# Kernel tuning notes

Measured on AMD Instinct MI355X. Metric: run time of the kernel, lower is better.

## Reference

```python
import math
import jax, jax.numpy as jnp
import numpy as np

B, T, D = 2, 2048, 1024
NUM_HEADS = 16
NUM_KV_HEADS = 4
HEAD_DIM = 64
ROPE_THETA = 500000.0


def precompute_freqs_cis(dim, seq_len, theta):
    freqs = 1.0 / theta ** (jnp.arange(0, dim, 2).astype(jnp.float32) / dim)
    freqs = jnp.outer(jnp.arange(seq_len), freqs)  # [T, dim//2]
    return jnp.cos(freqs), jnp.sin(freqs)


def apply_rotary_emb(xq, xk, cos, sin):
    # xq:[B,T,H,Dh], cos/sin:[T,Dh//2] -> broadcast as [1,T,1,Dh//2]
    c = cos[None, :, None, :]
    s = sin[None, :, None, :]

    def rot(x):
        xr = x.reshape(*x.shape[:-1], -1, 2)
        x0, x1 = xr[..., 0], xr[..., 1]
        return jnp.stack([x0 * c - x1 * s, x1 * c + x0 * s], axis=-1).reshape(x.shape)

    return rot(xq), rot(xk)


def setup_inputs() -> dict:
    key = jax.random.key(0)
    ks = jax.random.split(key, 5)
    x = jax.random.normal(ks[0], (B, T, D), dtype=jnp.float32)
    # causal mask [B,1,T,T]
    mask = jnp.broadcast_to(jnp.tril(jnp.ones((T, T), dtype=bool))[None, None], (B, 1, T, T))
    sq = 1.0 / math.sqrt(D)
    Wq = jax.random.normal(ks[1], (D, NUM_HEADS * HEAD_DIM), dtype=jnp.float32) * sq
    Wk = jax.random.normal(ks[2], (D, NUM_KV_HEADS * HEAD_DIM), dtype=jnp.float32) * sq
    Wv = jax.random.normal(ks[3], (D, NUM_KV_HEADS * HEAD_DIM), dtype=jnp.float32) * sq
    Wo = jax.random.normal(ks[4], (NUM_HEADS * HEAD_DIM, D), dtype=jnp.float32) * (1.0 / math.sqrt(NUM_HEADS * HEAD_DIM))
    return {"x": x, "mask": mask, "Wq": Wq, "Wk": Wk, "Wv": Wv, "Wo": Wo}


def reference(x, mask, Wq, Wk, Wv, Wo):
    b, t, _ = x.shape
    n_rep = NUM_HEADS // NUM_KV_HEADS
    q = (x @ Wq).reshape(b, t, NUM_HEADS, HEAD_DIM)
    k = (x @ Wk).reshape(b, t, NUM_KV_HEADS, HEAD_DIM)
    v = (x @ Wv).reshape(b, t, NUM_KV_HEADS, HEAD_DIM)
    cos, sin = precompute_freqs_cis(HEAD_DIM, t, ROPE_THETA)
    q, k = apply_rotary_emb(q, k, cos, sin)
    k = jnp.repeat(k, n_rep, axis=2)
    v = jnp.repeat(v, n_rep, axis=2)
    q = q.transpose(0, 2, 1, 3)  # [B,H,T,Dh]
    k = k.transpose(0, 2, 1, 3)
    v = v.transpose(0, 2, 1, 3)
    scale = 1.0 / math.sqrt(HEAD_DIM)
    attn = jnp.einsum('bhqd,bhkd->bhqk', q, k) * scale
    attn = jnp.where(mask, attn, -1e9)
    attn = jax.nn.softmax(attn, axis=-1)
    out = jnp.einsum('bhqk,bhkd->bhqd', attn, v)
    out = out.transpose(0, 2, 1, 3).reshape(b, t, -1)
    return out @ Wo
```

## Files before the change

kernel.cpp:

```cpp
#include <hip/hip_runtime.h>
#include <hip/hip_bf16.h>

#define B_  2
#define T_  2048
#define D_  1024
#define H_  16
#define KH_ 4
#define DH_ 64

typedef __attribute__((ext_vector_type(8))) short bf16x8;
typedef __attribute__((ext_vector_type(4))) float f32x4;

#define QSCALE 0.18033688011112043f

#if defined(__has_builtin)
#  if __has_builtin(__builtin_amdgcn_exp2f)
#    define EXP2F(x) __builtin_amdgcn_exp2f(x)
#  endif
#endif
#ifndef EXP2F
#  define EXP2F(x) exp2f(x)
#endif

__device__ __forceinline__ unsigned short f2bf(float f) {
  union { float f; unsigned int u; } v; v.f = f;
  return (unsigned short)((v.u + 0x7FFFu + ((v.u >> 16) & 1u)) >> 16);
}
__device__ __forceinline__ unsigned int pk2(float a, float b) {
  union { __hip_bfloat162 h2; unsigned int u; } v;
  v.h2 = __float22bfloat162_rn(make_float2(a, b));
  return v.u;
}


__global__ __launch_bounds__(256) void prep_kernel(
    const float* __restrict__ x,  const float* __restrict__ Wq,
    const float* __restrict__ Wk, const float* __restrict__ Wv,
    const float* __restrict__ Wo,
    short* __restrict__ xb, short* __restrict__ WT, short* __restrict__ WoT,
    float2* __restrict__ tbl) {
  __shared__ short Ts[64 * 72];
  const int bid = blockIdx.x, tid = threadIdx.x;

  if (bid < 2048) {
    const size_t i8 = ((size_t)bid * 256 + tid) * 8;
    const float4 a = *(const float4*)&x[i8];
    const float4 b = *(const float4*)&x[i8 + 4];
    uint4 p; p.x = pk2(a.x, a.y); p.y = pk2(a.z, a.w);
    p.z = pk2(b.x, b.y); p.w = pk2(b.z, b.w);
    *(uint4*)&xb[i8] = p;
  } else if (bid < 2688) {
    const bool isW = bid < 2432;
    const int idx = isW ? (bid - 2048) : (bid - 2432);
    const int n0 = (idx >> 4) * 64, k0 = (idx & 15) * 64;
    const float* src; int ncols, c0; short* dst;
    if (isW) {
      dst = WT;
      if (n0 < 1024)      { src = Wq; ncols = 1024; c0 = n0; }
      else if (n0 < 1280) { src = Wk; ncols = 256;  c0 = n0 - 1024; }
      else                { src = Wv; ncols = 256;  c0 = n0 - 1280; }
    } else { dst = WoT; src = Wo; ncols = 1024; c0 = n0; }
    for (int i = tid; i < 1024; i += 256) {
      const int kr = i >> 4, c4 = (i & 15) << 2;
      const int kc = isW ? kr : ((kr & 15) * 4 + (kr >> 4));
      const float4 w = *(const float4*)&src[(size_t)(k0 + kr) * ncols + c0 + c4];
      Ts[(c4 + 0) * 72 + kc] = (short)f2bf(w.x);
      Ts[(c4 + 1) * 72 + kc] = (short)f2bf(w.y);
      Ts[(c4 + 2) * 72 + kc] = (short)f2bf(w.z);
      Ts[(c4 + 3) * 72 + kc] = (short)f2bf(w.w);
    }
    __syncthreads();
    for (int c = tid; c < 512; c += 256) {
      const int nr = c >> 3, c8 = (c & 7) * 8;
      *(bf16x8*)&dst[(size_t)(n0 + nr) * 1024 + k0 + c8] =
          *(const bf16x8*)&Ts[nr * 72 + c8];
    }
  } else {
    const int e = (bid - 2688) * 256 + tid;
    const int t = e >> 5, i2 = e & 31;
    const float freq = exp2f(-(float)(2 * i2) * (18.931568569324174f / 64.0f));
    float sn, cs; sincosf((float)t * freq, &sn, &cs);
    tbl[e] = make_float2(cs, sn);
  }
}

__global__ __launch_bounds__(256) void qkv_mfma_kernel(
    const short* __restrict__ xb, const short* __restrict__ WT,
    const float2* __restrict__ tbl,
    short* __restrict__ qo, short* __restrict__ ko, short* __restrict__ vt) {
  __shared__ short Xs[128 * 136];
  __shared__ short Wt[64 * 136];
  const int tid = threadIdx.x;
  const int lane = tid & 63, w = tid >> 6;
  const int lm = lane & 15, quad = lane >> 4;
  const int m0 = blockIdx.x * 128;
  const int n0 = blockIdx.y * 64;

  f32x4 acc[2][4];
  #pragma unroll
  for (int sm = 0; sm < 2; ++sm)
    #pragma unroll
    for (int ct = 0; ct < 4; ++ct) acc[sm][ct] = (f32x4){0.f, 0.f, 0.f, 0.f};

  bf16x8 px[8], pw[4];
  #pragma unroll
  for (int u = 0; u < 8; ++u) {
    const int c = tid + u * 256, row = c >> 4, c8 = (c & 15) * 8;
    px[u] = *(const bf16x8*)&xb[(size_t)(m0 + row) * 1024 + c8];
  }
  #pragma unroll
  for (int u = 0; u < 4; ++u) {
    const int c = tid + u * 256, row = c >> 4, c8 = (c & 15) * 8;
    pw[u] = *(const bf16x8*)&WT[(size_t)(n0 + row) * 1024 + c8];
  }

  for (int kt = 0; kt < 8; ++kt) {
    __syncthreads();
    #pragma unroll
    for (int u = 0; u < 8; ++u) {
      const int c = tid + u * 256, row = c >> 4, c8 = (c & 15) * 8;
      *(bf16x8*)&Xs[row * 136 + c8] = px[u];
    }
    #pragma unroll
    for (int u = 0; u < 4; ++u) {
      const int c = tid + u * 256, row = c >> 4, c8 = (c & 15) * 8;
      *(bf16x8*)&Wt[row * 136 + c8] = pw[u];
    }
    __syncthreads();
    if (kt < 7) {
      #pragma unroll
      for (int u = 0; u < 8; ++u) {
        const int c = tid + u * 256, row = c >> 4, c8 = (c & 15) * 8;
        px[u] = *(const bf16x8*)&xb[(size_t)(m0 + row) * 1024 + (kt + 1) * 128 + c8];
      }
      #pragma unroll
      for (int u = 0; u < 4; ++u) {
        const int c = tid + u * 256, row = c >> 4, c8 = (c & 15) * 8;
        pw[u] = *(const bf16x8*)&WT[(size_t)(n0 + row) * 1024 + (kt + 1) * 128 + c8];
      }
    }
    #pragma unroll
    for (int s = 0; s < 4; ++s) {
      bf16x8 bfr[4];
      #pragma unroll
      for (int ct = 0; ct < 4; ++ct)
        bfr[ct] = *(const bf16x8*)&Wt[(ct * 16 + lm) * 136 + s * 32 + quad * 8];
      #pragma unroll
      for (int sm = 0; sm < 2; ++sm) {
        const bf16x8 a =
            *(const bf16x8*)&Xs[(w * 32 + sm * 16 + lm) * 136 + s * 32 + quad * 8];
        #pragma unroll
        for (int ct = 0; ct < 4; ++ct)
          acc[sm][ct] =
              __builtin_amdgcn_mfma_f32_16x16x32_bf16(a, bfr[ct], acc[sm][ct], 0, 0, 0);
      }
    }
  }

  if (n0 < 1280) {
    const bool isQ = n0 < 1024;
    short* outp = isQ ? qo : ko;
    const int base = isQ ? n0 : n0 - 1024;
    const int nh = isQ ? H_ : KH_;
    const int hh = base >> 6;
    const float post = isQ ? QSCALE : 1.0f;
    #pragma unroll
    for (int sm = 0; sm < 2; ++sm)
      #pragma unroll
      for (int r = 0; r < 4; ++r) {
        const int row = m0 + w * 32 + sm * 16 + quad * 4 + r;
        const int b = row >> 11, t = row & 2047;
        float v4[4];
        #pragma unroll
        for (int ct = 0; ct < 4; ++ct) {
          float val = acc[sm][ct][r];
          const float other = __shfl_xor(val, 1);
          const int ci = ct * 16 + lm;
          const float2 cs = tbl[t * 32 + (ci >> 1)];
          val = ((ci & 1) == 0) ? (val * cs.x - other * cs.y)
                                : (val * cs.x + other * cs.y);
          v4[ct] = val * post;
        }
        uint2 st; st.x = pk2(v4[0], v4[1]); st.y = pk2(v4[2], v4[3]);
        *(uint2*)&outp[((size_t)(b * nh + hh) * T_ + t) * DH_ + lm * 4] = st;
      }
  } else {
    __syncthreads();
    #pragma unroll
    for (int sm = 0; sm < 2; ++sm)
      #pragma unroll
      for (int r = 0; r < 4; ++r)
        #pragma unroll
        for (int ct = 0; ct < 4; ++ct)
          Xs[(w * 32 + sm * 16 + quad * 4 + r) * 72 + ct * 16 + lm] =
              (short)f2bf(acc[sm][ct][r]);
    __syncthreads();
    const int kh = (n0 - 1280) >> 6;
    const int b = m0 >> 11, t0 = m0 & 2047;
    short* vb = vt + (size_t)(b * KH_ + kh) * DH_ * T_;
    for (int c = tid; c < 1024; c += 256) {
      const int d = c >> 4, c8 = (c & 15) * 8;
      short tmp[8];
      #pragma unroll
      for (int j = 0; j < 8; ++j) {
        const int s = c8 + j, sg = s & 63;
        const int tok = (s & 64) + ((sg & 3) << 4) + (sg >> 2);
        tmp[j] = Xs[tok * 72 + d];
      }
      *(bf16x8*)&vb[(size_t)d * T_ + t0 + c8] = *(bf16x8*)tmp;
    }
  }
}

__global__ __launch_bounds__(256) void attn_mfma_kernel(
    const short* __restrict__ q, const short* __restrict__ k,
    const short* __restrict__ vt, short* __restrict__ att) {
  __shared__ short Qs[64 * 72];
  __shared__ short Ks[128 * 72];
  __shared__ short Vts[64 * 136];
  __shared__ short Ps0[64 * 72];
  __shared__ short Ps1[64 * 72];

  const int h = blockIdx.y, b = blockIdx.z;
  const int kh = h >> 2;
  const int tid = threadIdx.x;
  const int lane = tid & 63, w = tid >> 6;
  const int lm = lane & 15, quad = lane >> 4;

  const short* qb = q + (size_t)(b * H_ + h) * T_ * DH_;
  const short* kb = k + (size_t)(b * KH_ + kh) * T_ * DH_;
  const short* vb = vt + (size_t)(b * KH_ + kh) * DH_ * T_;

  bf16x8 ones;
  #pragma unroll
  for (int i = 0; i < 8; ++i) ones[i] = (short)0x3F80;

  for (int half = 0; half < 2; ++half) {
    const int qt = half ? (31 - blockIdx.x) : blockIdx.x;
    const int q0 = qt * 64;

    __syncthreads();
    for (int c = tid; c < 512; c += 256) {
      const int row = c >> 3, c8 = (c & 7) * 8;
      *(bf16x8*)&Qs[row * 72 + c8] =
          *(const bf16x8*)&qb[(size_t)(q0 + row) * 64 + c8];
    }

    bf16x8 pk[4], pv[4];
    #pragma unroll
    for (int u = 0; u < 4; ++u) {
      const int c = tid + u * 256;
      const int row = c >> 3, c8 = (c & 7) * 8;
      pk[u] = *(const bf16x8*)&kb[(size_t)row * 64 + c8];
      const int d = c >> 4, c16 = (c & 15) * 8;
      pv[u] = *(const bf16x8*)&vb[(size_t)d * T_ + c16];
    }
    __syncthreads();
    bf16x8 aq[2];
    #pragma unroll
    for (int s = 0; s < 2; ++s)
      aq[s] = *(const bf16x8*)&Qs[(w * 16 + lm) * 72 + s * 32 + quad * 8];

    f32x4 oacc[4], lacc;
    #pragma unroll
    for (int i = 0; i < 4; ++i) oacc[i] = (f32x4){0.f, 0.f, 0.f, 0.f};
    lacc = (f32x4){0.f, 0.f, 0.f, 0.f};

    auto step = [&](int j, bool diag, short* Ps) {
      f32x4 sacc[4];
      #pragma unroll
      for (int i = 0; i < 4; ++i) sacc[i] = (f32x4){0.f, 0.f, 0.f, 0.f};
      #pragma unroll
      for (int s = 0; s < 2; ++s) {
        #pragma unroll
        for (int ct = 0; ct < 4; ++ct) {
          const bf16x8 bb =
              *(const bf16x8*)&Ks[(j * 64 + ct * 16 + lm) * 72 + s * 32 + quad * 8];
          sacc[ct] = __builtin_amdgcn_mfma_f32_16x16x32_bf16(aq[s], bb, sacc[ct], 0, 0, 0);
        }
      }
      if (diag) {
        #pragma unroll
        for (int r = 0; r < 4; ++r) {
          const int qi = w * 16 + quad * 4 + r;
          float p[4];
          #pragma unroll
          for (int ct = 0; ct < 4; ++ct) {
            float pv2 = EXP2F(sacc[ct][r]);
            if ((ct * 16 + lm) > qi) pv2 = 0.f;
            p[ct] = pv2;
          }
          uint2 pw2; pw2.x = pk2(p[0], p[1]); pw2.y = pk2(p[2], p[3]);
          *(uint2*)&Ps[qi * 72 + lm * 4] = pw2;
        }
      } else {
        #pragma unroll
        for (int r = 0; r < 4; ++r) {
          const int qi = w * 16 + quad * 4 + r;
          uint2 pw2;
          pw2.x = pk2(EXP2F(sacc[0][r]), EXP2F(sacc[1][r]));
          pw2.y = pk2(EXP2F(sacc[2][r]), EXP2F(sacc[3][r]));
          *(uint2*)&Ps[qi * 72 + lm * 4] = pw2;
        }
      }
      #pragma unroll
      for (int s = 0; s < 2; ++s) {
        const bf16x8 pa = *(const bf16x8*)&Ps[(w * 16 + lm) * 72 + s * 32 + quad * 8];
        lacc = __builtin_amdgcn_mfma_f32_16x16x32_bf16(pa, ones, lacc, 0, 0, 0);
        #pragma unroll
        for (int ct = 0; ct < 4; ++ct) {
          const bf16x8 vfr = *(const bf16x8*)&Vts[(ct * 16 + lm) * 136 +
                                                  j * 64 + s * 32 + quad * 8];
          oacc[ct] = __builtin_amdgcn_mfma_f32_16x16x32_bf16(pa, vfr, oacc[ct], 0, 0, 0);
        }
      }
    };

    auto stage = [&](int r2) {
      __syncthreads();
      #pragma unroll
      for (int u = 0; u < 4; ++u) {
        const int c = tid + u * 256;
        const int row = c >> 3, c8 = (c & 7) * 8;
        *(bf16x8*)&Ks[row * 72 + c8] = pk[u];
        const int d = c >> 4, c16 = (c & 15) * 8;
        *(bf16x8*)&Vts[d * 136 + c16] = pv[u];
      }
      __syncthreads();
      const int r2n = (r2 + 2 <= 30) ? (r2 + 2) : 30;
      #pragma unroll
      for (int u = 0; u < 4; ++u) {
        const int c = tid + u * 256;
        const int row = c >> 3, c8 = (c & 7) * 8;
        pk[u] = *(const bf16x8*)&kb[(size_t)(r2n * 64 + row) * 64 + c8];
        const int d = c >> 4, c16 = (c & 15) * 8;
        pv[u] = *(const bf16x8*)&vb[(size_t)d * T_ + r2n * 64 + c16];
      }
    };

    int r2 = 0;
    for (; r2 + 1 <= qt; r2 += 2) {
      stage(r2);
      step(0, false, Ps0);
      step(1, r2 + 1 == qt, Ps1);
    }
    if (r2 == qt) {
      stage(r2);
      step(0, true, Ps0);
    }

    #pragma unroll
    for (int r = 0; r < 4; ++r) {
      const int qrow = q0 + w * 16 + quad * 4 + r;
      const float inv = 1.f / lacc[r];
      uint2 st;
      st.x = pk2(oacc[0][r] * inv, oacc[1][r] * inv);
      st.y = pk2(oacc[2][r] * inv, oacc[3][r] * inv);
      *(uint2*)&att[((size_t)b * T_ + qrow) * 1024 + h * 64 + lm * 4] = st;
    }
  }
}

__global__ __launch_bounds__(256) void outproj_mfma_kernel(
    const short* __restrict__ att, const short* __restrict__ WoT,
    float* __restrict__ out) {
  __shared__ short Xs[128 * 136];
  __shared__ short Wt[64 * 136];
  const int tid = threadIdx.x;
  const int lane = tid & 63, w = tid >> 6;
  const int lm = lane & 15, quad = lane >> 4;
  const int m0 = blockIdx.x * 128;
  const int n0 = blockIdx.y * 64;

  f32x4 acc[2][4];
  #pragma unroll
  for (int sm = 0; sm < 2; ++sm)
    #pragma unroll
    for (int ct = 0; ct < 4; ++ct) acc[sm][ct] = (f32x4){0.f, 0.f, 0.f, 0.f};

  bf16x8 px[8], pw[4];
  #pragma unroll
  for (int u = 0; u < 8; ++u) {
    const int c = tid + u * 256, row = c >> 4, c8 = (c & 15) * 8;
    px[u] = *(const bf16x8*)&att[(size_t)(m0 + row) * 1024 + c8];
  }
  #pragma unroll
  for (int u = 0; u < 4; ++u) {
    const int c = tid + u * 256, row = c >> 4, c8 = (c & 15) * 8;
    pw[u] = *(const bf16x8*)&WoT[(size_t)(n0 + row) * 1024 + c8];
  }

  for (int kt = 0; kt < 8; ++kt) {
    __syncthreads();
    #pragma unroll
    for (int u = 0; u < 8; ++u) {
      const int c = tid + u * 256, row = c >> 4, c8 = (c & 15) * 8;
      *(bf16x8*)&Xs[row * 136 + c8] = px[u];
    }
    #pragma unroll
    for (int u = 0; u < 4; ++u) {
      const int c = tid + u * 256, row = c >> 4, c8 = (c & 15) * 8;
      *(bf16x8*)&Wt[row * 136 + c8] = pw[u];
    }
    __syncthreads();
    if (kt < 7) {
      #pragma unroll
      for (int u = 0; u < 8; ++u) {
        const int c = tid + u * 256, row = c >> 4, c8 = (c & 15) * 8;
        px[u] = *(const bf16x8*)&att[(size_t)(m0 + row) * 1024 + (kt + 1) * 128 + c8];
      }
      #pragma unroll
      for (int u = 0; u < 4; ++u) {
        const int c = tid + u * 256, row = c >> 4, c8 = (c & 15) * 8;
        pw[u] = *(const bf16x8*)&WoT[(size_t)(n0 + row) * 1024 + (kt + 1) * 128 + c8];
      }
    }
    #pragma unroll
    for (int s = 0; s < 4; ++s) {
      bf16x8 bfr[4];
      #pragma unroll
      for (int ct = 0; ct < 4; ++ct)
        bfr[ct] = *(const bf16x8*)&Wt[(ct * 16 + lm) * 136 + s * 32 + quad * 8];
      #pragma unroll
      for (int sm = 0; sm < 2; ++sm) {
        const bf16x8 a =
            *(const bf16x8*)&Xs[(w * 32 + sm * 16 + lm) * 136 + s * 32 + quad * 8];
        #pragma unroll
        for (int ct = 0; ct < 4; ++ct)
          acc[sm][ct] =
              __builtin_amdgcn_mfma_f32_16x16x32_bf16(a, bfr[ct], acc[sm][ct], 0, 0, 0);
      }
    }
  }

  #pragma unroll
  for (int sm = 0; sm < 2; ++sm)
    #pragma unroll
    for (int r = 0; r < 4; ++r) {
      const int row = m0 + w * 32 + sm * 16 + quad * 4 + r;
      #pragma unroll
      for (int ct = 0; ct < 4; ++ct)
        out[(size_t)row * 1024 + n0 + ct * 16 + lm] = acc[sm][ct][r];
    }
}

extern "C" void kernel_launch(void* const* d_in, const int* in_sizes, int n_in,
                              void* d_out, int out_size, void* d_ws, size_t ws_size,
                              hipStream_t stream) {
  const float* x  = (const float*)d_in[0];
  const float* Wq = (const float*)d_in[2];
  const float* Wk = (const float*)d_in[3];
  const float* Wv = (const float*)d_in[4];
  const float* Wo = (const float*)d_in[5];
  float* out = (float*)d_out;

  short* xb   = (short*)d_ws;
  short* WT   = xb  + (size_t)4194304;
  short* WoT  = WT  + (size_t)1572864;
  short* qb   = WoT + (size_t)1048576;
  short* kb   = qb  + (size_t)4194304;
  short* vtb  = kb  + (size_t)1048576;
  short* attb = vtb + (size_t)1048576;
  float2* tbl = (float2*)(attb + (size_t)4194304);

  prep_kernel<<<dim3(2944), dim3(256), 0, stream>>>(
      x, Wq, Wk, Wv, Wo, xb, WT, WoT, tbl);
  qkv_mfma_kernel<<<dim3(32, 24), dim3(256), 0, stream>>>(xb, WT, tbl, qb, kb, vtb);
  attn_mfma_kernel<<<dim3(16, H_, B_), dim3(256), 0, stream>>>(qb, kb, vtb, attb);
  outproj_mfma_kernel<<<dim3(32, 16), dim3(256), 0, stream>>>(attb, WoT, out);
}
```

Before: 173.0 us.

## Use direct global-to-LDS loads with XOR swizzle and reschedule attention grid

The QKV and output-projection GEMMs now load tiles with global_load_lds straight into an XOR-swizzled, unpadded shared buffer instead of staging through registers. This removes the register prefetch, and with it the overlap of the next tile's loads with compute, because each k-step waits on vmcnt(0). The attention kernel drops the paired-query-tile loop and instead launches one block per query tile on a flat 1024-block grid ordered heaviest-first. It also loads Q fragments directly from global, and adds s_setprio around MFMA sections to favor matrix issue across waves.

```diff
diff --git a/kernel.cpp b/kernel.cpp
--- a/kernel.cpp
+++ b/kernel.cpp
@@ -30,6 +30,12 @@
   union { __hip_bfloat162 h2; unsigned int u; } v;
   v.h2 = __float22bfloat162_rn(make_float2(a, b));
   return v.u;
+}
+
+__device__ __forceinline__ void g2l16(const void* g, void* l) {
+  __builtin_amdgcn_global_load_lds(
+      (const __attribute__((address_space(1))) void*)g,
+      (__attribute__((address_space(3))) void*)l, 16, 0, 0);
 }
 
 
@@ -88,11 +94,13 @@
     const short* __restrict__ xb, const short* __restrict__ WT,
     const float2* __restrict__ tbl,
     short* __restrict__ qo, short* __restrict__ ko, short* __restrict__ vt) {
-  __shared__ short Xs[128 * 136];
-  __shared__ short Wt[64 * 136];
+  __shared__ short Xs[128 * 128];
+  __shared__ short Wt[64 * 128];
   const int tid = threadIdx.x;
   const int lane = tid & 63, w = tid >> 6;
   const int lm = lane & 15, quad = lane >> 4;
+  const int lr = lane >> 4;
+  const int lb = lane & 15;
   const int m0 = blockIdx.x * 128;
   const int n0 = blockIdx.y * 64;
 
@@ -102,53 +110,35 @@
     #pragma unroll
     for (int ct = 0; ct < 4; ++ct) acc[sm][ct] = (f32x4){0.f, 0.f, 0.f, 0.f};
 
-  bf16x8 px[8], pw[4];
-  #pragma unroll
-  for (int u = 0; u < 8; ++u) {
-    const int c = tid + u * 256, row = c >> 4, c8 = (c & 15) * 8;
-    px[u] = *(const bf16x8*)&xb[(size_t)(m0 + row) * 1024 + c8];
-  }
-  #pragma unroll
-  for (int u = 0; u < 4; ++u) {
-    const int c = tid + u * 256, row = c >> 4, c8 = (c & 15) * 8;
-    pw[u] = *(const bf16x8*)&WT[(size_t)(n0 + row) * 1024 + c8];
-  }
-
   for (int kt = 0; kt < 8; ++kt) {
     __syncthreads();
     #pragma unroll
     for (int u = 0; u < 8; ++u) {
-      const int c = tid + u * 256, row = c >> 4, c8 = (c & 15) * 8;
-      *(bf16x8*)&Xs[row * 136 + c8] = px[u];
+      const int r = (w * 8 + u) * 4 + lr;
+      const int sb = lb ^ (r & 7);
+      g2l16(&xb[(size_t)(m0 + r) * 1024 + kt * 128 + sb * 8],
+            &Xs[(w * 8 + u) * 512]);
     }
     #pragma unroll
     for (int u = 0; u < 4; ++u) {
-      const int c = tid + u * 256, row = c >> 4, c8 = (c & 15) * 8;
-      *(bf16x8*)&Wt[row * 136 + c8] = pw[u];
-    }
-    __syncthreads();
-    if (kt < 7) {
-      #pragma unroll
-      for (int u = 0; u < 8; ++u) {
-        const int c = tid + u * 256, row = c >> 4, c8 = (c & 15) * 8;
-        px[u] = *(const bf16x8*)&xb[(size_t)(m0 + row) * 1024 + (kt + 1) * 128 + c8];
-      }
-      #pragma unroll
-      for (int u = 0; u < 4; ++u) {
-        const int c = tid + u * 256, row = c >> 4, c8 = (c & 15) * 8;
-        pw[u] = *(const bf16x8*)&WT[(size_t)(n0 + row) * 1024 + (kt + 1) * 128 + c8];
-      }
-    }
+      const int r = (w * 4 + u) * 4 + lr;
+      const int sb = lb ^ (r & 7);
+      g2l16(&WT[(size_t)(n0 + r) * 1024 + kt * 128 + sb * 8],
+            &Wt[(w * 4 + u) * 512]);
+    }
+    asm volatile("s_waitcnt vmcnt(0)" ::: "memory");
+    __syncthreads();
     #pragma unroll
     for (int s = 0; s < 4; ++s) {
       bf16x8 bfr[4];
       #pragma unroll
       for (int ct = 0; ct < 4; ++ct)
-        bfr[ct] = *(const bf16x8*)&Wt[(ct * 16 + lm) * 136 + s * 32 + quad * 8];
+        bfr[ct] = *(const bf16x8*)&Wt[(ct * 16 + lm) * 128 +
+                                      (((s * 4 + quad) ^ (lm & 7)) << 3)];
       #pragma unroll
       for (int sm = 0; sm < 2; ++sm) {
-        const bf16x8 a =
-            *(const bf16x8*)&Xs[(w * 32 + sm * 16 + lm) * 136 + s * 32 + quad * 8];
+        const bf16x8 a = *(const bf16x8*)&Xs[(w * 32 + sm * 16 + lm) * 128 +
+                                             (((s * 4 + quad) ^ (lm & 7)) << 3)];
         #pragma unroll
         for (int ct = 0; ct < 4; ++ct)
           acc[sm][ct] =
@@ -215,17 +205,20 @@
 __global__ __launch_bounds__(256) void attn_mfma_kernel(
     const short* __restrict__ q, const short* __restrict__ k,
     const short* __restrict__ vt, short* __restrict__ att) {
-  __shared__ short Qs[64 * 72];
   __shared__ short Ks[128 * 72];
   __shared__ short Vts[64 * 136];
   __shared__ short Ps0[64 * 72];
   __shared__ short Ps1[64 * 72];
 
-  const int h = blockIdx.y, b = blockIdx.z;
+  const int bx = blockIdx.x;
+  const int qt = 31 - (bx >> 5);
+  const int hb = bx & 31;
+  const int h = hb >> 1, b = hb & 1;
   const int kh = h >> 2;
   const int tid = threadIdx.x;
   const int lane = tid & 63, w = tid >> 6;
   const int lm = lane & 15, quad = lane >> 4;
+  const int q0 = qt * 64;
 
   const short* qb = q + (size_t)(b * H_ + h) * T_ * DH_;
   const short* kb = k + (size_t)(b * KH_ + kh) * T_ * DH_;
@@ -235,140 +228,134 @@
   #pragma unroll
   for (int i = 0; i < 8; ++i) ones[i] = (short)0x3F80;
 
-  for (int half = 0; half < 2; ++half) {
-    const int qt = half ? (31 - blockIdx.x) : blockIdx.x;
-    const int q0 = qt * 64;
-
-    __syncthreads();
-    for (int c = tid; c < 512; c += 256) {
-      const int row = c >> 3, c8 = (c & 7) * 8;
-      *(bf16x8*)&Qs[row * 72 + c8] =
-          *(const bf16x8*)&qb[(size_t)(q0 + row) * 64 + c8];
-    }
-
-    bf16x8 pk[4], pv[4];
+  bf16x8 aq[2];
+  #pragma unroll
+  for (int s = 0; s < 2; ++s)
+    aq[s] = *(const bf16x8*)&qb[(size_t)(q0 + w * 16 + lm) * 64 + s * 32 + quad * 8];
+
+  bf16x8 pk[4], pv[4];
+  #pragma unroll
+  for (int u = 0; u < 4; ++u) {
+    const int c = tid + u * 256;
+    const int row = c >> 3, c8 = (c & 7) * 8;
+    pk[u] = *(const bf16x8*)&kb[(size_t)row * 64 + c8];
+    const int d = c >> 4, c16 = (c & 15) * 8;
+    pv[u] = *(const bf16x8*)&vb[(size_t)d * T_ + c16];
+  }
+
+  f32x4 oacc[4], lacc;
+  #pragma unroll
+  for (int i = 0; i < 4; ++i) oacc[i] = (f32x4){0.f, 0.f, 0.f, 0.f};
+  lacc = (f32x4){0.f, 0.f, 0.f, 0.f};
+
+  auto step = [&](int j, bool diag, short* Ps) {
+    f32x4 sacc[4];
+    #pragma unroll
+    for (int i = 0; i < 4; ++i) sacc[i] = (f32x4){0.f, 0.f, 0.f, 0.f};
+    __builtin_amdgcn_s_setprio(1);
+    #pragma unroll
+    for (int s = 0; s < 2; ++s) {
+      #pragma unroll
+      for (int ct = 0; ct < 4; ++ct) {
+        const bf16x8 bb =
+            *(const bf16x8*)&Ks[(j * 64 + ct * 16 + lm) * 72 + s * 32 + quad * 8];
+        sacc[ct] = __builtin_amdgcn_mfma_f32_16x16x32_bf16(aq[s], bb, sacc[ct], 0, 0, 0);
+      }
+    }
+    __builtin_amdgcn_s_setprio(0);
+    if (diag) {
+      #pragma unroll
+      for (int r = 0; r < 4; ++r) {
+        const int qi = w * 16 + quad * 4 + r;
+        float p[4];
+        #pragma unroll
+        for (int ct = 0; ct < 4; ++ct) {
+          float pv2 = EXP2F(sacc[ct][r]);
+          if ((ct * 16 + lm) > qi) pv2 = 0.f;
+          p[ct] = pv2;
+        }
+        uint2 pw2; pw2.x = pk2(p[0], p[1]); pw2.y = pk2(p[2], p[3]);
+        *(uint2*)&Ps[qi * 72 + lm * 4] = pw2;
+      }
+    } else {
+      #pragma unroll
+      for (int r = 0; r < 4; ++r) {
+        const int qi = w * 16 + quad * 4 + r;
+        uint2 pw2;
+        pw2.x = pk2(EXP2F(sacc[0][r]), EXP2F(sacc[1][r]));
+        pw2.y = pk2(EXP2F(sacc[2][r]), EXP2F(sacc[3][r]));
+        *(uint2*)&Ps[qi * 72 + lm * 4] = pw2;
+      }
+    }
+    __builtin_amdgcn_s_setprio(1);
+    #pragma unroll
+    for (int s = 0; s < 2; ++s) {
+      const bf16x8 pa = *(const bf16x8*)&Ps[(w * 16 + lm) * 72 + s * 32 + quad * 8];
+      lacc = __builtin_amdgcn_mfma_f32_16x16x32_bf16(pa, ones, lacc, 0, 0, 0);
+      #pragma unroll
+      for (int ct = 0; ct < 4; ++ct) {
+        const bf16x8 vfr = *(const bf16x8*)&Vts[(ct * 16 + lm) * 136 +
+                                                j * 64 + s * 32 + quad * 8];
+        oacc[ct] = __builtin_amdgcn_mfma_f32_16x16x32_bf16(pa, vfr, oacc[ct], 0, 0, 0);
+      }
+    }
+    __builtin_amdgcn_s_setprio(0);
+  };
+
+  auto stage = [&](int r2) {
+    __syncthreads();
     #pragma unroll
     for (int u = 0; u < 4; ++u) {
       const int c = tid + u * 256;
       const int row = c >> 3, c8 = (c & 7) * 8;
-      pk[u] = *(const bf16x8*)&kb[(size_t)row * 64 + c8];
+      *(bf16x8*)&Ks[row * 72 + c8] = pk[u];
       const int d = c >> 4, c16 = (c & 15) * 8;
-      pv[u] = *(const bf16x8*)&vb[(size_t)d * T_ + c16];
-    }
-    __syncthreads();
-    bf16x8 aq[2];
-    #pragma unroll
-    for (int s = 0; s < 2; ++s)
-      aq[s] = *(const bf16x8*)&Qs[(w * 16 + lm) * 72 + s * 32 + quad * 8];
-
-    f32x4 oacc[4], lacc;
-    #pragma unroll
-    for (int i = 0; i < 4; ++i) oacc[i] = (f32x4){0.f, 0.f, 0.f, 0.f};
-    lacc = (f32x4){0.f, 0.f, 0.f, 0.f};
-
-    auto step = [&](int j, bool diag, short* Ps) {
-      f32x4 sacc[4];
-      #pragma unroll
-      for (int i = 0; i < 4; ++i) sacc[i] = (f32x4){0.f, 0.f, 0.f, 0.f};
-      #pragma unroll
-      for (int s = 0; s < 2; ++s) {
-        #pragma unroll
-        for (int ct = 0; ct < 4; ++ct) {
-          const bf16x8 bb =
-              *(const bf16x8*)&Ks[(j * 64 + ct * 16 + lm) * 72 + s * 32 + quad * 8];
-          sacc[ct] = __builtin_amdgcn_mfma_f32_16x16x32_bf16(aq[s], bb, sacc[ct], 0, 0, 0);
-        }
-      }
-      if (diag) {
-        #pragma unroll
-        for (int r = 0; r < 4; ++r) {
-          const int qi = w * 16 + quad * 4 + r;
-          float p[4];
-          #pragma unroll
-          for (int ct = 0; ct < 4; ++ct) {
-            float pv2 = EXP2F(sacc[ct][r]);
-            if ((ct * 16 + lm) > qi) pv2 = 0.f;
-            p[ct] = pv2;
-          }
-          uint2 pw2; pw2.x = pk2(p[0], p[1]); pw2.y = pk2(p[2], p[3]);
-          *(uint2*)&Ps[qi * 72 + lm * 4] = pw2;
-        }
-      } else {
-        #pragma unroll
-        for (int r = 0; r < 4; ++r) {
-          const int qi = w * 16 + quad * 4 + r;
-          uint2 pw2;
-          pw2.x = pk2(EXP2F(sacc[0][r]), EXP2F(sacc[1][r]));
-          pw2.y = pk2(EXP2F(sacc[2][r]), EXP2F(sacc[3][r]));
-          *(uint2*)&Ps[qi * 72 + lm * 4] = pw2;
-        }
-      }
-      #pragma unroll
-      for (int s = 0; s < 2; ++s) {
-        const bf16x8 pa = *(const bf16x8*)&Ps[(w * 16 + lm) * 72 + s * 32 + quad * 8];
-        lacc = __builtin_amdgcn_mfma_f32_16x16x32_bf16(pa, ones, lacc, 0, 0, 0);
-        #pragma unroll
-        for (int ct = 0; ct < 4; ++ct) {
-          const bf16x8 vfr = *(const bf16x8*)&Vts[(ct * 16 + lm) * 136 +
-                                                  j * 64 + s * 32 + quad * 8];
-          oacc[ct] = __builtin_amdgcn_mfma_f32_16x16x32_bf16(pa, vfr, oacc[ct], 0, 0, 0);
-        }
-      }
-    };
-
-    auto stage = [&](int r2) {
-      __syncthreads();
-      #pragma unroll
-      for (int u = 0; u < 4; ++u) {
-        const int c = tid + u * 256;
-        const int row = c >> 3, c8 = (c & 7) * 8;
-        *(bf16x8*)&Ks[row * 72 + c8] = pk[u];
-        const int d = c >> 4, c16 = (c & 15) * 8;
-        *(bf16x8*)&Vts[d * 136 + c16] = pv[u];
-      }
-      __syncthreads();
-      const int r2n = (r2 + 2 <= 30) ? (r2 + 2) : 30;
-      #pragma unroll
-      for (int u = 0; u < 4; ++u) {
-        const int c = tid + u * 256;
-        const int row = c >> 3, c8 = (c & 7) * 8;
-        pk[u] = *(const bf16x8*)&kb[(size_t)(r2n * 64 + row) * 64 + c8];
-        const int d = c >> 4, c16 = (c & 15) * 8;
-        pv[u] = *(const bf16x8*)&vb[(size_t)d * T_ + r2n * 64 + c16];
-      }
-    };
-
-    int r2 = 0;
-    for (; r2 + 1 <= qt; r2 += 2) {
-      stage(r2);
-      step(0, false, Ps0);
-      step(1, r2 + 1 == qt, Ps1);
-    }
-    if (r2 == qt) {
-      stage(r2);
-      step(0, true, Ps0);
-    }
-
-    #pragma unroll
-    for (int r = 0; r < 4; ++r) {
-      const int qrow = q0 + w * 16 + quad * 4 + r;
-      const float inv = 1.f / lacc[r];
-      uint2 st;
-      st.x = pk2(oacc[0][r] * inv, oacc[1][r] * inv);
-      st.y = pk2(oacc[2][r] * inv, oacc[3][r] * inv);
-      *(uint2*)&att[((size_t)b * T_ + qrow) * 1024 + h * 64 + lm * 4] = st;
-    }
+      *(bf16x8*)&Vts[d * 136 + c16] = pv[u];
+    }
+    __syncthreads();
+    const int r2n = (r2 + 2 <= qt) ? (r2 + 2) : r2;
+    #pragma unroll
+    for (int u = 0; u < 4; ++u) {
+      const int c = tid + u * 256;
+      const int row = c >> 3, c8 = (c & 7) * 8;
+      pk[u] = *(const bf16x8*)&kb[(size_t)(r2n * 64 + row) * 64 + c8];
+      const int d = c >> 4, c16 = (c & 15) * 8;
+      pv[u] = *(const bf16x8*)&vb[(size_t)d * T_ + r2n * 64 + c16];
+    }
+  };
+
+  int r2 = 0;
+  for (; r2 + 1 <= qt; r2 += 2) {
+    stage(r2);
+    step(0, false, Ps0);
+    step(1, r2 + 1 == qt, Ps1);
+  }
+  if (r2 == qt) {
+    stage(r2);
+    step(0, true, Ps0);
+  }
+
+  #pragma unroll
+  for (int r = 0; r < 4; ++r) {
+    const int qrow = q0 + w * 16 + quad * 4 + r;
+    const float inv = 1.f / lacc[r];
+    uint2 st;
+    st.x = pk2(oacc[0][r] * inv, oacc[1][r] * inv);
+    st.y = pk2(oacc[2][r] * inv, oacc[3][r] * inv);
+    *(uint2*)&att[((size_t)b * T_ + qrow) * 1024 + h * 64 + lm * 4] = st;
   }
 }
 
 __global__ __launch_bounds__(256) void outproj_mfma_kernel(
     const short* __restrict__ att, const short* __restrict__ WoT,
     float* __restrict__ out) {
-  __shared__ short Xs[128 * 136];
-  __shared__ short Wt[64 * 136];
+  __shared__ short Xs[128 * 128];
+  __shared__ short Wt[64 * 128];
   const int tid = threadIdx.x;
   const int lane = tid & 63, w = tid >> 6;
   const int lm = lane & 15, quad = lane >> 4;
+  const int lr = lane >> 4;
+  const int lb = lane & 15;
   const int m0 = blockIdx.x * 128;
   const int n0 = blockIdx.y * 64;
 
@@ -378,53 +365,35 @@
     #pragma unroll
     for (int ct = 0; ct < 4; ++ct) acc[sm][ct] = (f32x4){0.f, 0.f, 0.f, 0.f};
 
-  bf16x8 px[8], pw[4];
-  #pragma unroll
-  for (int u = 0; u < 8; ++u) {
-    const int c = tid + u * 256, row = c >> 4, c8 = (c & 15) * 8;
-    px[u] = *(const bf16x8*)&att[(size_t)(m0 + row) * 1024 + c8];
-  }
-  #pragma unroll
-  for (int u = 0; u < 4; ++u) {
-    const int c = tid + u * 256, row = c >> 4, c8 = (c & 15) * 8;
-    pw[u] = *(const bf16x8*)&WoT[(size_t)(n0 + row) * 1024 + c8];
-  }
-
   for (int kt = 0; kt < 8; ++kt) {
     __syncthreads();
     #pragma unroll
     for (int u = 0; u < 8; ++u) {
-      const int c = tid + u * 256, row = c >> 4, c8 = (c & 15) * 8;
-      *(bf16x8*)&Xs[row * 136 + c8] = px[u];
+      const int r = (w * 8 + u) * 4 + lr;
+      const int sb = lb ^ (r & 7);
+      g2l16(&att[(size_t)(m0 + r) * 1024 + kt * 128 + sb * 8],
+            &Xs[(w * 8 + u) * 512]);
     }
     #pragma unroll
     for (int u = 0; u < 4; ++u) {
-      const int c = tid + u * 256, row = c >> 4, c8 = (c & 15) * 8;
-      *(bf16x8*)&Wt[row * 136 + c8] = pw[u];
-    }
-    __syncthreads();
-    if (kt < 7) {
-      #pragma unroll
-      for (int u = 0; u < 8; ++u) {
-        const int c = tid + u * 256, row = c >> 4, c8 = (c & 15) * 8;
-        px[u] = *(const bf16x8*)&att[(size_t)(m0 + row) * 1024 + (kt + 1) * 128 + c8];
-      }
-      #pragma unroll
-      for (int u = 0; u < 4; ++u) {
-        const int c = tid + u * 256, row = c >> 4, c8 = (c & 15) * 8;
-        pw[u] = *(const bf16x8*)&WoT[(size_t)(n0 + row) * 1024 + (kt + 1) * 128 + c8];
-      }
-    }
+      const int r = (w * 4 + u) * 4 + lr;
+      const int sb = lb ^ (r & 7);
+      g2l16(&WoT[(size_t)(n0 + r) * 1024 + kt * 128 + sb * 8],
+            &Wt[(w * 4 + u) * 512]);
+    }
+    asm volatile("s_waitcnt vmcnt(0)" ::: "memory");
+    __syncthreads();
     #pragma unroll
     for (int s = 0; s < 4; ++s) {
       bf16x8 bfr[4];
       #pragma unroll
       for (int ct = 0; ct < 4; ++ct)
-        bfr[ct] = *(const bf16x8*)&Wt[(ct * 16 + lm) * 136 + s * 32 + quad * 8];
+        bfr[ct] = *(const bf16x8*)&Wt[(ct * 16 + lm) * 128 +
+                                      (((s * 4 + quad) ^ (lm & 7)) << 3)];
       #pragma unroll
       for (int sm = 0; sm < 2; ++sm) {
-        const bf16x8 a =
-            *(const bf16x8*)&Xs[(w * 32 + sm * 16 + lm) * 136 + s * 32 + quad * 8];
+        const bf16x8 a = *(const bf16x8*)&Xs[(w * 32 + sm * 16 + lm) * 128 +
+                                             (((s * 4 + quad) ^ (lm & 7)) << 3)];
         #pragma unroll
         for (int ct = 0; ct < 4; ++ct)
           acc[sm][ct] =
@@ -466,6 +435,6 @@
   prep_kernel<<<dim3(2944), dim3(256), 0, stream>>>(
       x, Wq, Wk, Wv, Wo, xb, WT, WoT, tbl);
   qkv_mfma_kernel<<<dim3(32, 24), dim3(256), 0, stream>>>(xb, WT, tbl, qb, kb, vtb);
-  attn_mfma_kernel<<<dim3(16, H_, B_), dim3(256), 0, stream>>>(qb, kb, vtb, attb);
+  attn_mfma_kernel<<<dim3(1024), dim3(256), 0, stream>>>(qb, kb, vtb, attb);
   outproj_mfma_kernel<<<dim3(32, 16), dim3(256), 0, stream>>>(attb, WoT, out);
 }
```

Result: no change. 174.8 us (+1.1%).
